# Performance work log

Hardware: AMD Instinct MI355X
Metric: run time of the kernel (lower is better)

## Reference

```python
import jax, jax.numpy as jnp
import numpy as np

T, H = 8192, 2048
E, K = 16, 4
I_MOE = 1408
I_SHARED = 5632
SCALE = 0.02  # keep activations numerically sane (source uses randn init)


def setup_inputs() -> dict:
    key = jax.random.key(0)
    ks = jax.random.split(key, 8)
    return {
        "hidden_states": jax.random.normal(ks[0], (T, H), jnp.float32),
        "router_w": jax.random.normal(ks[1], (E, H), jnp.float32) * SCALE,
        "gate_up_w": jax.random.normal(ks[2], (E, H, 2 * I_MOE), jnp.float32) * SCALE,
        "down_w": jax.random.normal(ks[3], (E, I_MOE, H), jnp.float32) * SCALE,
        "shared_gate_w": jax.random.normal(ks[4], (H, I_SHARED), jnp.float32) * SCALE,
        "shared_up_w": jax.random.normal(ks[5], (H, I_SHARED), jnp.float32) * SCALE,
        "shared_down_w": jax.random.normal(ks[6], (I_SHARED, H), jnp.float32) * SCALE,
        "shared_expert_gate_w": jax.random.normal(ks[7], (H, 1), jnp.float32) * SCALE,
    }


def reference(hidden_states, router_w, gate_up_w, down_w,
              shared_gate_w, shared_up_w, shared_down_w, shared_expert_gate_w):
    t, h = hidden_states.shape
    e = router_w.shape[0]
    # --- Router: fp32 logits -> softmax -> top-k ---
    logits = hidden_states.astype(jnp.float32) @ router_w.T            # [T, E]
    probs = jax.nn.softmax(logits, axis=-1)
    routing_weights, routing_indices = jax.lax.top_k(probs, K)         # [T, K]
    # --- Dispatch: replicate each token K times, sort replicas by expert ---
    flat_experts = routing_indices.reshape(-1)                          # [T*K]
    perm = jnp.argsort(flat_experts)                                    # stable sort
    dispatched = hidden_states[perm // K]                               # [T*K, H]
    group_sizes = jnp.bincount(flat_experts, length=e).astype(jnp.int32)
    # --- Grouped GEMM experts (SwiGLU) ---
    merged = jax.lax.ragged_dot(dispatched, gate_up_w, group_sizes)     # [T*K, 2I]
    gate, up = jnp.split(merged, 2, axis=-1)
    act = jax.nn.silu(gate) * up                                        # [T*K, I]
    expert_out = jax.lax.ragged_dot(act, down_w, group_sizes)           # [T*K, H]
    # --- Unpermute + weighted combine ---
    inv = jnp.argsort(perm)
    replica_out = expert_out[inv].reshape(t, K, h)                      # [T, K, H]
    out = jnp.einsum('tk,tkh->th', routing_weights, replica_out)
    # --- Shared expert with sigmoid gate ---
    shared = (jax.nn.silu(hidden_states @ shared_gate_w)
              * (hidden_states @ shared_up_w)) @ shared_down_w          # [T, H]
    g = jax.nn.sigmoid(hidden_states @ shared_expert_gate_w)            # [T, 1]
    return out + g * shared
```

## Files before the change

### kernel.cpp

```cpp
#include <hip/hip_runtime.h>
#include <hip/hip_bf16.h>

#define T_TOK 8192
#define H_DIM 2048
#define NE    16
#define TOPK  4
#define IMOE  1408
#define ISH   5632
#define TK    (T_TOK*TOPK)
#define MAXT256 ((TK/256)+NE)

typedef __bf16 bf16;
typedef __attribute__((ext_vector_type(8))) __bf16 bf16x8;
typedef __attribute__((ext_vector_type(4))) float  f32x4;

__device__ __forceinline__ void gload_lds16(const bf16* g, bf16* l) {
  __builtin_amdgcn_global_load_lds((const __attribute__((address_space(1))) void*)g,
                                   (__attribute__((address_space(3))) void*)l, 16, 0, 0);
}
#define MEMFENCE asm volatile("" ::: "memory")
#define BARRIER  do { MEMFENCE; __builtin_amdgcn_s_barrier(); MEMFENCE; } while (0)
#define VMCNT4   asm volatile("s_waitcnt vmcnt(4)" ::: "memory")

__global__ __launch_bounds__(256) void cvt_transpose64(const float* __restrict__ in,
                                                       bf16* __restrict__ out,
                                                       int R, int C,
                                                       size_t strideIn, size_t strideOut,
                                                       int split, int base_off) {
  __shared__ float tile[64][65];
  const float* inm = in + (size_t)blockIdx.z * strideIn;
  bf16* outm = out + (size_t)blockIdx.z * strideOut;
  int c0 = blockIdx.x * 64, r0 = blockIdx.y * 64;
  int tid = threadIdx.x;
  int rr = tid >> 4, cc4 = (tid & 15) * 4;
  #pragma unroll
  for (int i = 0; i < 4; ++i) {
    f32x4 v = __builtin_nontemporal_load(
        (const f32x4*)&inm[(size_t)(r0 + rr + i * 16) * C + c0 + cc4]);
    tile[rr + i * 16][cc4 + 0] = v.x;
    tile[rr + i * 16][cc4 + 1] = v.y;
    tile[rr + i * 16][cc4 + 2] = v.z;
    tile[rr + i * 16][cc4 + 3] = v.w;
  }
  __syncthreads();
  int r8 = (tid & 7) * 8;
  #pragma unroll
  for (int i = 0; i < 2; ++i) {
    int c = (tid >> 3) + i * 32;
    int co = c0 + c;
    int orow;
    if (split < 0) orow = co;
    else {
      int cl = co, o = base_off;
      if (cl >= split) { cl -= split; o += 128; }
      orow = ((cl >> 7) << 8) + o + (cl & 127);
    }
    bf16x8 v;
    #pragma unroll
    for (int j = 0; j < 8; ++j) v[j] = (bf16)tile[r8 + j][c];
    *(bf16x8*)&outm[(size_t)orow * R + r0 + r8] = v;
  }
}

__global__ void init_kernel(int* counts, int* fill) {
  int i = threadIdx.x;
  if (i < NE) { counts[i] = 0; fill[i] = 0; }
}

__global__ __launch_bounds__(256) void router_kernel(const float* __restrict__ X,
                                                     const float* __restrict__ Wr,
                                                     const float* __restrict__ wgate,
                                                     bf16* __restrict__ Xbf,
                                                     float* __restrict__ topk_w,
                                                     int* __restrict__ topk_idx,
                                                     float* __restrict__ gate_sig) {
  const int wv = threadIdx.x >> 6, lane = threadIdx.x & 63;
  const int t = blockIdx.x * 4 + wv;
  const float* x = X + (size_t)t * H_DIM;
  float xf[32];
  #pragma unroll
  for (int j = 0; j < 32; ++j) xf[j] = x[j * 64 + lane];
  #pragma unroll
  for (int j = 0; j < 32; ++j) Xbf[(size_t)t * H_DIM + j * 64 + lane] = (bf16)xf[j];

  double lg = 0.0;
  for (int e = 0; e < NE + 1; ++e) {
    const float* w = (e < NE) ? (Wr + (size_t)e * H_DIM) : wgate;
    double s0 = 0.0, s1 = 0.0;
    #pragma unroll
    for (int j = 0; j < 32; j += 2) {
      s0 += (double)xf[j] * (double)w[j * 64 + lane];
      s1 += (double)xf[j + 1] * (double)w[(j + 1) * 64 + lane];
    }
    double s = s0 + s1;
    #pragma unroll
    for (int off = 32; off; off >>= 1) s += __shfl_xor(s, off);
    if (lane == e) lg = s;
  }

  double v = (lane < NE) ? lg : -1e300;
  double m = v;
  #pragma unroll
  for (int off = 32; off; off >>= 1) m = fmax(m, __shfl_xor(m, off));
  double ev = (lane < NE) ? exp(v - m) : 0.0;
  double den = ev;
  #pragma unroll
  for (int off = 32; off; off >>= 1) den += __shfl_xor(den, off);

  double vv = v;
  int widx = 0; double wval = 0.0;
  for (int k = 0; k < TOPK; ++k) {
    double bv = vv; int bi = lane;
    #pragma unroll
    for (int off = 32; off; off >>= 1) {
      double ov = __shfl_xor(bv, off);
      int oi = __shfl_xor(bi, off);
      if (ov > bv || (ov == bv && oi < bi)) { bv = ov; bi = oi; }
    }
    double evb = __shfl(ev, bi);
    if (lane == k) { widx = bi; wval = evb / den; }
    if (lane == bi) vv = -1e300;
  }
  if (lane < TOPK) {
    topk_idx[t * TOPK + lane] = widx;
    topk_w[t * TOPK + lane] = (float)wval;
  }
  if (lane == NE) gate_sig[t] = (float)(1.0 / (1.0 + exp(-lg)));
}

__global__ __launch_bounds__(256) void hist_kernel(const int* __restrict__ tidx,
                                                   int* __restrict__ counts) {
  __shared__ int h[NE];
  if (threadIdx.x < NE) h[threadIdx.x] = 0;
  __syncthreads();
  int gid = blockIdx.x * 256 + threadIdx.x;
  atomicAdd(&h[tidx[gid]], 1);
  __syncthreads();
  if (threadIdx.x < NE) atomicAdd(&counts[threadIdx.x], h[threadIdx.x]);
}

__global__ void scan_kernel(const int* __restrict__ counts, int* __restrict__ offs,
                            int* __restrict__ fill, int* __restrict__ ttab,
                            int* __restrict__ ntl) {
  if (threadIdx.x != 0) return;
  int off = 0;
  for (int e = 0; e < NE; ++e) { offs[e] = off; off += counts[e]; fill[e] = 0; }
  offs[NE] = off;
  int n = 0;
  for (int e = 0; e < NE; ++e) {
    int cnt = counts[e], end_ = offs[e] + cnt;
    for (int m = 0; m < cnt; m += 256) {
      ttab[n * 3 + 0] = e;
      ttab[n * 3 + 1] = offs[e] + m;
      ttab[n * 3 + 2] = end_;
      ++n;
    }
  }
  *ntl = n;
}

__global__ __launch_bounds__(256) void scatter_kernel(const int* __restrict__ topk_idx,
                                                      const int* __restrict__ offs,
                                                      int* __restrict__ fill,
                                                      int* __restrict__ row_token,
                                                      int* __restrict__ row_pos) {
  __shared__ int wc[4][NE];
  __shared__ int wbase[4][NE];
  __shared__ int bbase[NE];
  const int tid = threadIdx.x, wv = tid >> 6, lane = tid & 63;
  const int gid = blockIdx.x * 256 + tid;
  const int e = topk_idx[gid];
  int rank = 0;
  #pragma unroll
  for (int ex = 0; ex < NE; ++ex) {
    unsigned long long b = __ballot(e == ex);
    if (e == ex) rank = __popcll(b & ((1ull << lane) - 1));
    if (lane == 0) wc[wv][ex] = __popcll(b);
  }
  __syncthreads();
  if (tid < NE) {
    int s = 0;
    #pragma unroll
    for (int w = 0; w < 4; ++w) { wbase[w][tid] = s; s += wc[w][tid]; }
    bbase[tid] = atomicAdd(&fill[tid], s);
  }
  __syncthreads();
  int pos = offs[e] + bbase[e] + wbase[wv][e] + rank;
  row_token[pos] = gid >> 2;
  row_pos[gid] = pos;
}

__device__ __forceinline__ void mfma_cluster(f32x4 (&a)[4][2], bf16x8 (&A)[4][2],
                                             bf16x8 (&B)[2][2]) {
  __builtin_amdgcn_s_setprio(1);
  #pragma unroll
  for (int kk = 0; kk < 2; ++kk)
    #pragma unroll
    for (int m = 0; m < 4; ++m)
      #pragma unroll
      for (int n = 0; n < 2; ++n)
        a[m][n] = __builtin_amdgcn_mfma_f32_16x16x32_bf16(A[m][kk], B[n][kk], a[m][n], 0, 0, 0);
  __builtin_amdgcn_s_setprio(0);
}

struct GArgs {
  const bf16* A; const bf16* B; bf16* C;
  const int* row_token; const int* tile_tab; const int* n_tiles;
  size_t strideB;
  int lda, Ktot, ldc, Mdense, gx, gy;
};

__global__ __launch_bounds__(512, 2) void gemm256(GArgs ga, GArgs gb, int nblk0,
                                                  int fuse_swiglu) {
  GArgs g; int id;
  if ((int)blockIdx.x < nblk0) { g = ga; id = blockIdx.x; }
  else { g = gb; id = blockIdx.x - nblk0; }
  const int gx = g.gx, gy = g.gy;
  int mt, nt;
  if ((gx & 7) == 0) {
    int oct = id / (8 * gy);
    int rem = id - oct * 8 * gy;
    mt = oct * 8 + (rem & 7);
    nt = rem >> 3;
  } else {
    mt = id % gx;
    nt = id / gx;
  }

  int e, row_start, row_end;
  if (g.tile_tab) {
    if (mt >= *g.n_tiles) return;
    e = g.tile_tab[mt * 3 + 0];
    row_start = g.tile_tab[mt * 3 + 1];
    row_end = g.tile_tab[mt * 3 + 2];
  } else {
    e = 0; row_start = mt * 256; row_end = g.Mdense;
  }
  const bf16* Ap = g.A;
  const bf16* Bp = g.B + (size_t)e * g.strideB;
  const int lda = g.lda, Ktot = g.Ktot, ldc = g.ldc;
  bf16* C = g.C;

  __shared__ bf16 smA[2][2][8192];
  __shared__ bf16 smB[2][2][8192];

  const int tid = threadIdx.x;
  const int wave = tid >> 6;
  const int lane = tid & 63;

  unsigned aoff[2][2], boff[2][2];
  {
    int csrc = (((tid & 7) ^ ((tid >> 3) & 7)) << 3);
    #pragma unroll
    for (int h = 0; h < 2; ++h)
      #pragma unroll
      for (int j = 0; j < 2; ++j) {
        int rho = j * 64 + (tid >> 3);
        int r = row_start + h * 128 + rho;
        if (r > row_end - 1) r = row_end - 1;
        int sr = g.row_token ? g.row_token[r] : r;
        aoff[h][j] = (unsigned)sr * (unsigned)lda + (unsigned)csrc;
        boff[h][j] = (unsigned)(nt * 256 + h * 128 + rho) * (unsigned)Ktot + (unsigned)csrc;
      }
  }

  auto STAGE_A = [&](int bufi, int h, int tt) {
    gload_lds16(Ap + (size_t)(aoff[h][0] + (unsigned)tt * 64u), &smA[bufi][h][wave << 9]);
    gload_lds16(Ap + (size_t)(aoff[h][1] + (unsigned)tt * 64u), &smA[bufi][h][4096 + (wave << 9)]);
  };
  auto STAGE_B = [&](int bufi, int h, int tt) {
    gload_lds16(Bp + (size_t)(boff[h][0] + (unsigned)tt * 64u), &smB[bufi][h][wave << 9]);
    gload_lds16(Bp + (size_t)(boff[h][1] + (unsigned)tt * 64u), &smB[bufi][h][4096 + (wave << 9)]);
  };

  const int warow = ((wave >> 2) << 6) + (lane & 15);
  const int wbrow = ((wave & 3) << 5) + (lane & 15);
  const int q4 = lane >> 4;
  auto LDA_ = [&](int bufi, int h, int m, int kk) -> bf16x8 {
    int row = warow + m * 16;
    int c = (kk * 4 + q4) ^ (row & 7);
    return *(const bf16x8*)&smA[bufi][h][row * 64 + c * 8];
  };
  auto LDB_ = [&](int bufi, int h, int n, int kk) -> bf16x8 {
    int row = wbrow + n * 16;
    int c = (kk * 4 + q4) ^ (row & 7);
    return *(const bf16x8*)&smB[bufi][h][row * 64 + c * 8];
  };

  f32x4 acc[4][4][2];
  #pragma unroll
  for (int q = 0; q < 4; ++q)
    #pragma unroll
    for (int m = 0; m < 4; ++m)
      #pragma unroll
      for (int n = 0; n < 2; ++n) acc[q][m][n] = (f32x4){0.f, 0.f, 0.f, 0.f};

  bf16x8 Ar[4][2], Br0[2][2], Br1[2][2];

#define RD_A(BUF, H) do { \
    _Pragma("unroll") for (int m_ = 0; m_ < 4; ++m_) { \
      Ar[m_][0] = LDA_(BUF, H, m_, 0); Ar[m_][1] = LDA_(BUF, H, m_, 1); } } while (0)
#define RD_B(BUF, H, DST) do { \
    _Pragma("unroll") for (int n_ = 0; n_ < 2; ++n_) { \
      DST[n_][0] = LDB_(BUF, H, n_, 0); DST[n_][1] = LDB_(BUF, H, n_, 1); } } while (0)

#define DO_TILE(CB, NB, TS) do { \
     \
    RD_A(CB, 0); RD_B(CB, 0, Br0); \
    STAGE_A(NB, 0, TS); \
    BARRIER; \
    mfma_cluster(acc[0], Ar, Br0); \
    VMCNT4; \
    BARRIER; \
     \
    RD_B(CB, 1, Br1); \
    STAGE_B(NB, 0, TS); \
    BARRIER; \
    mfma_cluster(acc[1], Ar, Br1); \
    VMCNT4; \
    BARRIER; \
     \
    RD_A(CB, 1); \
    STAGE_B(NB, 1, TS); \
    BARRIER; \
    mfma_cluster(acc[2], Ar, Br1); \
    BARRIER; \
     \
    STAGE_A(NB, 1, TS); \
    mfma_cluster(acc[3], Ar, Br0); \
    VMCNT4; \
    BARRIER; \
  } while (0)

  STAGE_A(0, 0, 0); STAGE_B(0, 0, 0); STAGE_B(0, 1, 0); STAGE_A(0, 1, 0);
  VMCNT4; BARRIER;

  const int nk = Ktot >> 6;
  for (int it = 0; it < nk; it += 2) {
    const int ts1 = it + 1;
    const int ts2 = (it + 2 < nk) ? it + 2 : it + 1;
    DO_TILE(0, 1, ts1);
    DO_TILE(1, 0, ts2);
  }
#undef DO_TILE
#undef RD_A
#undef RD_B

  const int er = (lane >> 4) * 4;
  if (fuse_swiglu) {
    const int cb0 = nt * 128 + ((wave & 3) << 5) + (lane & 15);
    #pragma unroll
    for (int qi = 0; qi < 2; ++qi) {
      const int qg = qi ? 3 : 0, qu = qi ? 2 : 1;
      int rb = row_start + qi * 128 + ((wave >> 2) << 6) + er;
      #pragma unroll
      for (int m = 0; m < 4; ++m)
        #pragma unroll
        for (int n = 0; n < 2; ++n)
          #pragma unroll
          for (int j = 0; j < 4; ++j) {
            int r = rb + m * 16 + j;
            if (r < row_end) {
              float g0 = acc[qg][m][n][j];
              float u0 = acc[qu][m][n][j];
              float s = g0 / (1.f + __expf(-g0));
              C[(size_t)r * ldc + cb0 + n * 16] = (bf16)(s * u0);
            }
          }
    }
  } else {
    const int qr[4] = {0, 0, 1, 1}, qc[4] = {0, 1, 1, 0};
    #pragma unroll
    for (int q = 0; q < 4; ++q) {
      int rb = row_start + qr[q] * 128 + ((wave >> 2) << 6) + er;
      int cb0 = nt * 256 + qc[q] * 128 + ((wave & 3) << 5) + (lane & 15);
      #pragma unroll
      for (int m = 0; m < 4; ++m)
        #pragma unroll
        for (int n = 0; n < 2; ++n)
          #pragma unroll
          for (int j = 0; j < 4; ++j) {
            int r = rb + m * 16 + j;
            if (r < row_end) C[(size_t)r * ldc + cb0 + n * 16] = (bf16)acc[q][m][n][j];
          }
    }
  }
}

__global__ __launch_bounds__(256) void combine_kernel(const float* __restrict__ topk_w,
                                                      const int* __restrict__ row_pos,
                                                      const bf16* __restrict__ eout,
                                                      const bf16* __restrict__ shout,
                                                      const float* __restrict__ gate_sig,
                                                      float* __restrict__ out) {
  int t = blockIdx.x;
  float w0 = topk_w[t * 4 + 0], w1 = topk_w[t * 4 + 1];
  float w2 = topk_w[t * 4 + 2], w3 = topk_w[t * 4 + 3];
  size_t p0 = (size_t)row_pos[t * 4 + 0] * H_DIM;
  size_t p1 = (size_t)row_pos[t * 4 + 1] * H_DIM;
  size_t p2 = (size_t)row_pos[t * 4 + 2] * H_DIM;
  size_t p3 = (size_t)row_pos[t * 4 + 3] * H_DIM;
  float g = gate_sig[t];
  size_t tb = (size_t)t * H_DIM;
  size_t hb = (size_t)threadIdx.x * 8;
  bf16x8 a0 = *(const bf16x8*)&eout[p0 + hb];
  bf16x8 a1 = *(const bf16x8*)&eout[p1 + hb];
  bf16x8 a2 = *(const bf16x8*)&eout[p2 + hb];
  bf16x8 a3 = *(const bf16x8*)&eout[p3 + hb];
  bf16x8 sh = *(const bf16x8*)&shout[tb + hb];
  float r[8];
  #pragma unroll
  for (int j = 0; j < 8; ++j)
    r[j] = w0 * (float)a0[j] + w1 * (float)a1[j] + w2 * (float)a2[j]
         + w3 * (float)a3[j] + g * (float)sh[j];
  float4 o0 = {r[0], r[1], r[2], r[3]}, o1 = {r[4], r[5], r[6], r[7]};
  *(float4*)&out[tb + hb] = o0;
  *(float4*)&out[tb + hb + 4] = o1;
}

extern "C" void kernel_launch(void* const* d_in, const int* in_sizes, int n_in,
                              void* d_out, int out_size, void* d_ws, size_t ws_size,
                              hipStream_t stream) {
  const float* X   = (const float*)d_in[0];
  const float* Wr  = (const float*)d_in[1];
  const float* Wgu = (const float*)d_in[2];
  const float* Wd  = (const float*)d_in[3];
  const float* Wsg = (const float*)d_in[4];
  const float* Wsu = (const float*)d_in[5];
  const float* Wsd = (const float*)d_in[6];
  const float* Wge = (const float*)d_in[7];
  float* out = (float*)d_out;

  size_t off = 0;
  auto alloc = [&](size_t bytes) -> void* {
    void* p = (char*)d_ws + off;
    off += (bytes + 255) & ~(size_t)255;
    return p;
  };
  bf16* Xbf    = (bf16*)alloc((size_t)T_TOK * H_DIM * 2);
  bf16* WguT   = (bf16*)alloc((size_t)NE * 2 * IMOE * H_DIM * 2);
  bf16* WdT    = (bf16*)alloc((size_t)NE * H_DIM * IMOE * 2);
  bf16* WsguT  = (bf16*)alloc((size_t)2 * ISH * H_DIM * 2);
  bf16* WsdT   = (bf16*)alloc((size_t)H_DIM * ISH * 2);
  bf16* act    = (bf16*)alloc((size_t)TK * IMOE * 2);
  bf16* act_sh = (bf16*)alloc((size_t)T_TOK * ISH * 2);
  bf16* eout   = (bf16*)alloc((size_t)TK * H_DIM * 2);
  bf16* shout  = (bf16*)alloc((size_t)T_TOK * H_DIM * 2);
  float* tw    = (float*)alloc((size_t)T_TOK * TOPK * 4);
  int*   tidx  = (int*)alloc((size_t)T_TOK * TOPK * 4);
  float* gsig  = (float*)alloc((size_t)T_TOK * 4);
  int*   counts= (int*)alloc(64);
  int*   offs  = (int*)alloc(128);
  int*   fill  = (int*)alloc(64);
  int*   rowtok= (int*)alloc((size_t)TK * 4);
  int*   rowpos= (int*)alloc((size_t)TK * 4);
  int*   ttab  = (int*)alloc((size_t)MAXT256 * 3 * 4);
  int*   ntl   = (int*)alloc(64);
  if (off > ws_size) return;

  init_kernel<<<1, 32, 0, stream>>>(counts, fill);

  cvt_transpose64<<<dim3(H_DIM / 64, ISH / 64, 1), 256, 0, stream>>>(
      Wsd, WsdT, ISH, H_DIM, 0, 0, -1, 0);
  cvt_transpose64<<<dim3(ISH / 64, H_DIM / 64, 1), 256, 0, stream>>>(
      Wsg, WsguT, H_DIM, ISH, 0, 0, ISH, 0);
  cvt_transpose64<<<dim3(ISH / 64, H_DIM / 64, 1), 256, 0, stream>>>(
      Wsu, WsguT, H_DIM, ISH, 0, 0, ISH, 128);
  cvt_transpose64<<<dim3(H_DIM / 64, IMOE / 64, NE), 256, 0, stream>>>(
      Wd, WdT, IMOE, H_DIM, (size_t)IMOE * H_DIM, (size_t)IMOE * H_DIM, -1, 0);
  cvt_transpose64<<<dim3(2 * IMOE / 64, H_DIM / 64, NE), 256, 0, stream>>>(
      Wgu, WguT, H_DIM, 2 * IMOE, (size_t)H_DIM * 2 * IMOE, (size_t)H_DIM * 2 * IMOE, IMOE, 0);

  router_kernel<<<T_TOK / 4, 256, 0, stream>>>(X, Wr, Wge, Xbf, tw, tidx, gsig);
  hist_kernel<<<TK / 256, 256, 0, stream>>>(tidx, counts);
  scan_kernel<<<1, 64, 0, stream>>>(counts, offs, fill, ttab, ntl);
  scatter_kernel<<<TK / 256, 256, 0, stream>>>(tidx, offs, fill, rowtok, rowpos);

  GArgs g1;
  g1.A = Xbf; g1.B = WguT; g1.C = act;
  g1.row_token = rowtok; g1.tile_tab = ttab; g1.n_tiles = ntl;
  g1.strideB = (size_t)2 * IMOE * H_DIM;
  g1.lda = H_DIM; g1.Ktot = H_DIM; g1.ldc = IMOE; g1.Mdense = 0;
  g1.gx = MAXT256; g1.gy = 2 * IMOE / 256;
  GArgs gsg;
  gsg.A = Xbf; gsg.B = WsguT; gsg.C = act_sh;
  gsg.row_token = nullptr; gsg.tile_tab = nullptr; gsg.n_tiles = nullptr;
  gsg.strideB = 0;
  gsg.lda = H_DIM; gsg.Ktot = H_DIM; gsg.ldc = ISH; gsg.Mdense = T_TOK;
  gsg.gx = T_TOK / 256; gsg.gy = 2 * ISH / 256;
  int nb1 = g1.gx * g1.gy;
  gemm256<<<nb1 + gsg.gx * gsg.gy, 512, 0, stream>>>(g1, gsg, nb1, 1);

  GArgs g2;
  g2.A = act; g2.B = WdT; g2.C = eout;
  g2.row_token = nullptr; g2.tile_tab = ttab; g2.n_tiles = ntl;
  g2.strideB = (size_t)H_DIM * IMOE;
  g2.lda = IMOE; g2.Ktot = IMOE; g2.ldc = H_DIM; g2.Mdense = 0;
  g2.gx = MAXT256; g2.gy = H_DIM / 256;
  GArgs gsd;
  gsd.A = act_sh; gsd.B = WsdT; gsd.C = shout;
  gsd.row_token = nullptr; gsd.tile_tab = nullptr; gsd.n_tiles = nullptr;
  gsd.strideB = 0;
  gsd.lda = ISH; gsd.Ktot = ISH; gsd.ldc = H_DIM; gsd.Mdense = T_TOK;
  gsd.gx = T_TOK / 256; gsd.gy = H_DIM / 256;
  int nb2 = g2.gx * g2.gy;
  gemm256<<<nb2 + gsd.gx * gsd.gy, 512, 0, stream>>>(g2, gsd, nb2, 0);

  combine_kernel<<<T_TOK, 256, 0, stream>>>(tw, rowpos, eout, shout, gsig, out);
}
```

Measured before the change: 1.447 ms.

## Restructure GEMM K-loop pipeline to cut barriers and double-buffer A fragments

```diff
diff --git a/kernel.cpp b/kernel.cpp
--- a/kernel.cpp
+++ b/kernel.cpp
@@ -20,7 +20,8 @@
 }
 #define MEMFENCE asm volatile("" ::: "memory")
 #define BARRIER  do { MEMFENCE; __builtin_amdgcn_s_barrier(); MEMFENCE; } while (0)
-#define VMCNT4   asm volatile("s_waitcnt vmcnt(4)" ::: "memory")
+#define VMCNT2   asm volatile("s_waitcnt vmcnt(2)" ::: "memory")
+#define VMCNT0   asm volatile("s_waitcnt vmcnt(0)" ::: "memory")
 
 __global__ __launch_bounds__(256) void cvt_transpose64(const float* __restrict__ in,
                                                        bf16* __restrict__ out,
@@ -295,45 +296,43 @@
       #pragma unroll
       for (int n = 0; n < 2; ++n) acc[q][m][n] = (f32x4){0.f, 0.f, 0.f, 0.f};
 
-  bf16x8 Ar[4][2], Br0[2][2], Br1[2][2];
+  bf16x8 Ar[4][2], Ar2[4][2], Br0[2][2], Br1[2][2];
 
 #define RD_A(BUF, H) do { \
     _Pragma("unroll") for (int m_ = 0; m_ < 4; ++m_) { \
       Ar[m_][0] = LDA_(BUF, H, m_, 0); Ar[m_][1] = LDA_(BUF, H, m_, 1); } } while (0)
+#define RD_A2(BUF, H) do { \
+    _Pragma("unroll") for (int m_ = 0; m_ < 4; ++m_) { \
+      Ar2[m_][0] = LDA_(BUF, H, m_, 0); Ar2[m_][1] = LDA_(BUF, H, m_, 1); } } while (0)
 #define RD_B(BUF, H, DST) do { \
     _Pragma("unroll") for (int n_ = 0; n_ < 2; ++n_) { \
       DST[n_][0] = LDB_(BUF, H, n_, 0); DST[n_][1] = LDB_(BUF, H, n_, 1); } } while (0)
 
 #define DO_TILE(CB, NB, TS) do { \
      \
-    RD_A(CB, 0); RD_B(CB, 0, Br0); \
-    STAGE_A(NB, 0, TS); \
-    BARRIER; \
+    RD_A(CB, 0); RD_B(CB, 0, Br0); RD_B(CB, 1, Br1); \
+    STAGE_B(NB, 1, TS); \
     mfma_cluster(acc[0], Ar, Br0); \
-    VMCNT4; \
+    VMCNT2; \
     BARRIER; \
      \
-    RD_B(CB, 1, Br1); \
+    RD_A2(CB, 1); \
+    STAGE_A(NB, 0, TS); \
+    mfma_cluster(acc[1], Ar, Br1); \
+     \
     STAGE_B(NB, 0, TS); \
-    BARRIER; \
-    mfma_cluster(acc[1], Ar, Br1); \
-    VMCNT4; \
-    BARRIER; \
-     \
-    RD_A(CB, 1); \
-    STAGE_B(NB, 1, TS); \
-    BARRIER; \
-    mfma_cluster(acc[2], Ar, Br1); \
-    BARRIER; \
+    mfma_cluster(acc[2], Ar2, Br1); \
      \
     STAGE_A(NB, 1, TS); \
-    mfma_cluster(acc[3], Ar, Br0); \
-    VMCNT4; \
+    mfma_cluster(acc[3], Ar2, Br0); \
+    VMCNT2; \
     BARRIER; \
   } while (0)
 
-  STAGE_A(0, 0, 0); STAGE_B(0, 0, 0); STAGE_B(0, 1, 0); STAGE_A(0, 1, 0);
-  VMCNT4; BARRIER;
+  STAGE_A(0, 0, 0); STAGE_B(0, 0, 0); STAGE_B(0, 1, 0);
+  VMCNT0;
+  STAGE_A(0, 1, 0);
+  BARRIER;
 
   const int nk = Ktot >> 6;
   for (int it = 0; it < nk; it += 2) {
@@ -344,6 +343,7 @@
   }
 #undef DO_TILE
 #undef RD_A
+#undef RD_A2
 #undef RD_B
 
   const int er = (lane >> 4) * 4;
```

After: 1.763 ms. +21.8%, slower.
